# Optimization experiments

Hardware: AMD Instinct MI355X
Metric: run time of the kernel (lower is better)

The kernel has to match this reference:

```python
import jax, jax.numpy as jnp
import numpy as np

N = 8192
IOU_THRESH = 0.5
MAX_PROPOSALS = 1000


def setup_inputs() -> dict:
    key = jax.random.key(0)
    k1, k2, k3, k4 = jax.random.split(key, 4)
    # valid xyxy boxes inside a ~1000x1000 image, widths/heights in [1, 101)
    xy1 = jax.random.uniform(k1, (N, 2), dtype=jnp.float32) * 900.0
    wh = jax.random.uniform(k2, (N, 2), dtype=jnp.float32) * 100.0 + 1.0
    boxes = jnp.concatenate([xy1, xy1 + wh], axis=1)  # [N,4] xyxy
    scores = jax.random.uniform(k3, (N,), dtype=jnp.float32)
    return {"boxes": boxes, "scores": scores}


def _nms_keep(boxes, scores, thresh, max_proposals):
    # boxes: [N,4] xyxy (already sorted by descending score)
    x1, y1, x2, y2 = boxes[:, 0], boxes[:, 1], boxes[:, 2], boxes[:, 3]
    area = (x2 - x1) * (y2 - y1)  # [N]
    # pairwise IoU [N,N] (computed once; suppression loop gathers rows)
    xx1 = jnp.maximum(x1[:, None], x1[None, :])
    yy1 = jnp.maximum(y1[:, None], y1[None, :])
    xx2 = jnp.minimum(x2[:, None], x2[None, :])
    yy2 = jnp.minimum(y2[:, None], y2[None, :])
    inter = jnp.clip(xx2 - xx1, 0.0) * jnp.clip(yy2 - yy1, 0.0)
    iou = inter / (area[:, None] + area[None, :] - inter)
    n = boxes.shape[0]
    idx = jnp.arange(n)

    def body(i, keep):
        # box i (if still kept) suppresses later boxes with IoU > thresh
        suppress = keep[i] & (iou[i] > thresh) & (idx > i)
        return keep & ~suppress

    keep = jax.lax.fori_loop(0, n, body, jnp.ones((n,), dtype=bool))
    # truncate to max_proposals surviving boxes (in score order)
    keep = keep & (jnp.cumsum(keep.astype(jnp.int32)) <= max_proposals)
    return keep


def reference(boxes, scores):
    # sort by descending score (boxlist_nms sorts by score_field)
    order = jnp.argsort(-scores)
    b = boxes[order]          # [N,4]
    s = scores[order]         # [N]
    # keep mask is a discrete decision -> computed on stop_gradient inputs
    keep = _nms_keep(jax.lax.stop_gradient(b), jax.lax.stop_gradient(s),
                     IOU_THRESH, MAX_PROPOSALS)
    # fixed-shape output: [N,5] = (x1,y1,x2,y2,score), zeroed where suppressed
    out = jnp.concatenate([b, s[:, None]], axis=1) * keep[:, None].astype(b.dtype)
    return out
```

## Files before the change

### kernel.cpp

```cpp
#include <hip/hip_runtime.h>
#include <hip/hip_bf16.h>

#define N 8192
#define NW 128
#define GR 64
#define GROUPS 128
#define MAXP 1000
#define K_E 16
typedef unsigned long long u64;

__device__ float4 g_sboxes[N];
__device__ float  g_sscores[N];
__device__ u64    g_mask[(size_t)N * NW];
__device__ u64    g_diagT[N];
__device__ unsigned short g_elist[N][K_E];
__device__ int    g_ecnt[N];
__device__ u64    g_keep[NW];
__device__ int    g_wpre[NW];

__global__ __launch_bounds__(256) void k_rank2(const float4* __restrict__ boxes,
                                               const float* __restrict__ scores) {
  __shared__ u64 lk[8][1025];
  const int t = threadIdx.x;
  if (blockIdx.x < 32) g_ecnt[blockIdx.x * 256 + t] = 0;
#pragma unroll
  for (int k = 0; k < 32; ++k) {
    int j = t + 256 * k;
    unsigned sb = __float_as_uint(scores[j]);
    lk[j >> 10][j & 1023] = ((u64)(sb ^ 0xFFFFFFFFu) << 32) | (unsigned)j;
  }
  __syncthreads();
  const int row = blockIdx.x * 32 + (t >> 3);
  const int seg = t & 7;
  unsigned sbr = __float_as_uint(scores[row]);
  const u64 ki = ((u64)(sbr ^ 0xFFFFFFFFu) << 32) | (unsigned)row;
  const u64* s = lk[seg];
  int cnt = 0;
#pragma unroll 8
  for (int j = 0; j < 1024; ++j) cnt += (s[j] < ki) ? 1 : 0;
  cnt += __shfl_xor(cnt, 1);
  cnt += __shfl_xor(cnt, 2);
  cnt += __shfl_xor(cnt, 4);
  if (seg == 0) {
    g_sboxes[cnt] = boxes[row];
    g_sscores[cnt] = scores[row];
  }
}

__global__ __launch_bounds__(256) void k_mask4() {
#pragma clang fp contract(off)
  const int col = blockIdx.x;
  const int rowq = blockIdx.y;
  if (col < rowq * 4) return;
  const int t = threadIdx.x;
  const int wv = t >> 6, lane = t & 63;
  const int jbase = col * 64;
  __shared__ float4 cb[64];
  __shared__ u64 sh[4][64];
  if (t < 64) cb[t] = g_sboxes[jbase + t];
  __syncthreads();
  const int row = rowq * 4 + wv;
  if (col < row) return;
  const int i = row * 64 + lane;
  float4 bi = g_sboxes[i];
  u64 ov = 0;
  for (int c = 0; c < 64; ++c) {
    float4 bj = cb[c];
    float xx1 = fmaxf(bi.x, bj.x);
    float yy1 = fmaxf(bi.y, bj.y);
    float xx2 = fminf(bi.z, bj.z);
    float yy2 = fminf(bi.w, bj.w);
    bool cand = (xx2 > xx1) && (yy2 > yy1);
    if (cand) ov |= (1ull << c);
  }
  if (col == row) ov &= (lane < 63) ? (~0ull << (lane + 1)) : 0ull;
  float areai = (bi.z - bi.x) * (bi.w - bi.y);
  u64 bits = 0;
  while (ov) {
    int c = __ffsll((long long)ov) - 1;
    ov &= ov - 1;
    float4 bj = cb[c];
    float xx1 = fmaxf(bi.x, bj.x);
    float yy1 = fmaxf(bi.y, bj.y);
    float xx2 = fminf(bi.z, bj.z);
    float yy2 = fminf(bi.w, bj.w);
    float ww = fmaxf(xx2 - xx1, 0.0f);
    float hh = fmaxf(yy2 - yy1, 0.0f);
    float inter = ww * hh;
    float areaj = (bj.z - bj.x) * (bj.w - bj.y);
    float uni = (areai + areaj) - inter;
    float iou = inter / uni;
    if (iou > 0.5f) bits |= (1ull << c);
  }
  if (bits) g_mask[(size_t)i * NW + col] = bits;
  u64 eb = bits;
  while (eb) {
    int c = __ffsll((long long)eb) - 1;
    eb &= eb - 1;
    int slot = atomicAdd(&g_ecnt[i], 1);
    if (slot < K_E) g_elist[i][slot] = (unsigned short)(jbase + c);
  }
  if (col == row) {
    sh[wv][lane] = bits;
    u64 colw = 0;
    for (int r = 0; r < 64; ++r) colw |= ((sh[wv][r] >> lane) & 1ull) << r;
    g_diagT[row * 64 + lane] = colw;
  }
}

__global__ __launch_bounds__(64) void k_serial6() {
  const int lane = threadIdx.x;
  __shared__ u64 remv[NW];
  __shared__ u64 keep_arr[NW];
  remv[lane] = 0; remv[lane + 64] = 0;
  keep_arr[lane] = 0; keep_arr[lane + 64] = 0;

  u64 tdA = g_diagT[lane];
  int cnA = g_ecnt[lane];
  const u64* el0 = (const u64*)&g_elist[lane][0];
  u64 eA0 = el0[0], eA1 = el0[1], eA2 = el0[2], eA3 = el0[3];

  int kept_total = 0;
  for (int g = 0; g < GROUPS; ++g) {
    u64 tdB = 0, eB0 = 0, eB1 = 0, eB2 = 0, eB3 = 0;
    int cnB = 0;
    if (g + 1 < GROUPS) {
      int base = (g + 1) * GR + lane;
      tdB = g_diagT[base];
      cnB = g_ecnt[base];
      const u64* el = (const u64*)&g_elist[base][0];
      eB0 = el[0]; eB1 = el[1]; eB2 = el[2]; eB3 = el[3];
    }

    u64 pend = ~remv[g];
    u64 keepm = 0;
    while (pend) {
      bool rdy = (((pend >> lane) & 1ull) != 0ull) && ((tdA & pend) == 0ull);
      u64 R = __ballot(rdy);
      keepm |= R;
      u64 S = __ballot((tdA & R) != 0ull);
      pend &= ~(R | S);
    }
    if (lane == 0) keep_arr[g] = keepm;

    if ((keepm >> lane) & 1ull) {
      int cnt = cnA < K_E ? cnA : K_E;
      const u64 ew0 = eA0, ew1 = eA1, ew2 = eA2, ew3 = eA3;
#define SCAT(W, Q)                                                     \
      _Pragma("unroll")                                                \
      for (int b = 0; b < 4; ++b) {                                    \
        int s = (Q) * 4 + b;                                           \
        if (s < cnt) {                                                 \
          int j = (int)(((W) >> (16 * b)) & 0xFFFFull);                \
          atomicOr(&remv[j >> 6], 1ull << (j & 63));                   \
        }                                                              \
      }
      SCAT(ew0, 0) SCAT(ew1, 1) SCAT(ew2, 2) SCAT(ew3, 3)
#undef SCAT
    }
    u64 ovf = __ballot((((keepm >> lane) & 1ull) != 0ull) && (cnA > K_E));
    while (ovf) {
      int rr = __ffsll((long long)ovf) - 1;
      ovf &= ovf - 1;
      const u64* rowp = g_mask + (size_t)(g * GR + rr) * NW;
      int w0 = g + lane, w1 = g + 64 + lane;
      u64 a0 = (w0 < NW) ? rowp[w0] : 0ull;
      u64 a1 = (w1 < NW) ? rowp[w1] : 0ull;
      if (a0) atomicOr(&remv[w0], a0);
      if (a1) atomicOr(&remv[w1], a1);
    }

    kept_total += __popcll(keepm);
    if (kept_total >= MAXP) break;

    tdA = tdB; cnA = cnB;
    eA0 = eB0; eA1 = eB1; eA2 = eB2; eA3 = eB3;
  }

  u64 k0 = keep_arr[2 * lane];
  u64 k1 = keep_arr[2 * lane + 1];
  g_keep[2 * lane] = k0;
  g_keep[2 * lane + 1] = k1;
  int pc0 = __popcll(k0);
  int s = pc0 + __popcll(k1);
  int ex = s;
  for (int d = 1; d < 64; d <<= 1) {
    int t2 = __shfl_up(ex, d);
    if (lane >= d) ex += t2;
  }
  ex -= s;
  g_wpre[2 * lane] = ex;
  g_wpre[2 * lane + 1] = ex + pc0;
}

__global__ __launch_bounds__(256) void k_out(float* __restrict__ out) {
  int i = blockIdx.x * 256 + threadIdx.x;
  int w = i >> 6, b = i & 63;
  u64 kw = g_keep[w];
  int before = g_wpre[w] + (b ? __popcll(kw << (64 - b)) : 0);
  bool k = (((kw >> b) & 1ull) != 0ull) && (before < MAXP);
  float m = k ? 1.0f : 0.0f;
  float4 bx = g_sboxes[i];
  float sc = g_sscores[i];
  out[i * 5 + 0] = bx.x * m;
  out[i * 5 + 1] = bx.y * m;
  out[i * 5 + 2] = bx.z * m;
  out[i * 5 + 3] = bx.w * m;
  out[i * 5 + 4] = sc * m;
}

extern "C" void kernel_launch(void* const* d_in, const int* in_sizes, int n_in,
                              void* d_out, int out_size, void* d_ws, size_t ws_size,
                              hipStream_t stream) {
  const float4* boxes = (const float4*)d_in[0];
  const float*  scores = (const float*)d_in[1];
  float* out = (float*)d_out;

  hipLaunchKernelGGL(k_rank2,   dim3(N / 32),     dim3(256), 0, stream, boxes, scores);
  hipLaunchKernelGGL(k_mask4,   dim3(NW, NW / 4), dim3(256), 0, stream);
  hipLaunchKernelGGL(k_serial6, dim3(1),          dim3(64),  0, stream);
  hipLaunchKernelGGL(k_out,     dim3(N / 256),    dim3(256), 0, stream, out);
}
```

Measured before the change: 59.49 us.

## Compute mask for leading 48 groups first, fall back to full NMS only if needed

The IoU mask is first built only for the top 3072 score-sorted boxes, and the serial NMS runs over those groups. If 1000 boxes are kept within that prefix, the output is written directly. Otherwise a guarded full-mask kernel and full serial pass run as a fallback. The output write is also fused into the serial kernel, which drops the separate k_out launch. The cost is two extra launches that exit early, and a 256-thread single-block output loop in place of a 32-block grid.

```diff
diff --git a/kernel.cpp b/kernel.cpp
--- a/kernel.cpp
+++ b/kernel.cpp
@@ -5,6 +5,7 @@
 #define NW 128
 #define GR 64
 #define GROUPS 128
+#define CGR 48
 #define MAXP 1000
 #define K_E 16
 typedef unsigned long long u64;
@@ -13,16 +14,16 @@
 __device__ float  g_sscores[N];
 __device__ u64    g_mask[(size_t)N * NW];
 __device__ u64    g_diagT[N];
-__device__ unsigned short g_elist[N][K_E];
+__device__ __attribute__((aligned(8))) unsigned short g_elist[N][K_E];
 __device__ int    g_ecnt[N];
-__device__ u64    g_keep[NW];
-__device__ int    g_wpre[NW];
+__device__ int    g_need_full;
 
 __global__ __launch_bounds__(256) void k_rank2(const float4* __restrict__ boxes,
                                                const float* __restrict__ scores) {
   __shared__ u64 lk[8][1025];
   const int t = threadIdx.x;
   if (blockIdx.x < 32) g_ecnt[blockIdx.x * 256 + t] = 0;
+  if (blockIdx.x == 0 && t == 0) g_need_full = 0;
 #pragma unroll
   for (int k = 0; k < 32; ++k) {
     int j = t + 256 * k;
@@ -47,21 +48,11 @@
   }
 }
 
-__global__ __launch_bounds__(256) void k_mask4() {
+__device__ __forceinline__ void tile_work(int col, int row, int lane,
+                                          const float4* cb, u64* sh) {
 #pragma clang fp contract(off)
-  const int col = blockIdx.x;
-  const int rowq = blockIdx.y;
-  if (col < rowq * 4) return;
-  const int t = threadIdx.x;
-  const int wv = t >> 6, lane = t & 63;
+  const int i = row * 64 + lane;
   const int jbase = col * 64;
-  __shared__ float4 cb[64];
-  __shared__ u64 sh[4][64];
-  if (t < 64) cb[t] = g_sboxes[jbase + t];
-  __syncthreads();
-  const int row = rowq * 4 + wv;
-  if (col < row) return;
-  const int i = row * 64 + lane;
   float4 bi = g_sboxes[i];
   u64 ov = 0;
   for (int c = 0; c < 64; ++c) {
@@ -101,112 +92,159 @@
     if (slot < K_E) g_elist[i][slot] = (unsigned short)(jbase + c);
   }
   if (col == row) {
-    sh[wv][lane] = bits;
+    sh[lane] = bits;
     u64 colw = 0;
-    for (int r = 0; r < 64; ++r) colw |= ((sh[wv][r] >> lane) & 1ull) << r;
+    for (int r = 0; r < 64; ++r) colw |= ((sh[r] >> lane) & 1ull) << r;
     g_diagT[row * 64 + lane] = colw;
   }
 }
 
-__global__ __launch_bounds__(64) void k_serial6() {
-  const int lane = threadIdx.x;
+__global__ __launch_bounds__(256) void k_maskc() {
+  const int col = blockIdx.x;
+  const int rowq = blockIdx.y;
+  if (col < rowq * 4) return;
+  const int t = threadIdx.x;
+  const int wv = t >> 6, lane = t & 63;
+  __shared__ float4 cb[64];
+  __shared__ u64 sh[4][64];
+  if (t < 64) cb[t] = g_sboxes[col * 64 + t];
+  __syncthreads();
+  const int row = rowq * 4 + wv;
+  if (col < row) return;
+  tile_work(col, row, lane, cb, sh[wv]);
+}
+
+__global__ __launch_bounds__(256) void k_maskr() {
+  if (g_need_full == 0) return;
+  const int col = blockIdx.x;
+  const int rowq = blockIdx.y;
+  if (col < rowq * 4) return;
+  const int t = threadIdx.x;
+  const int wv = t >> 6, lane = t & 63;
+  __shared__ float4 cb[64];
+  __shared__ u64 sh[4][64];
+  if (t < 64) cb[t] = g_sboxes[col * 64 + t];
+  __syncthreads();
+  const int row = rowq * 4 + wv;
+  if (col < row) return;
+  if (row < CGR && col < CGR) return;
+  tile_work(col, row, lane, cb, sh[wv]);
+}
+
+template<int GLIM, bool GUARDED>
+__device__ __forceinline__ void serial_body(float* __restrict__ out) {
+  if (GUARDED && g_need_full == 0) return;
+  const int t = threadIdx.x;
+  const int wave = t >> 6, lane = t & 63;
   __shared__ u64 remv[NW];
   __shared__ u64 keep_arr[NW];
-  remv[lane] = 0; remv[lane + 64] = 0;
-  keep_arr[lane] = 0; keep_arr[lane + 64] = 0;
-
-  u64 tdA = g_diagT[lane];
-  int cnA = g_ecnt[lane];
-  const u64* el0 = (const u64*)&g_elist[lane][0];
-  u64 eA0 = el0[0], eA1 = el0[1], eA2 = el0[2], eA3 = el0[3];
-
-  int kept_total = 0;
-  for (int g = 0; g < GROUPS; ++g) {
-    u64 tdB = 0, eB0 = 0, eB1 = 0, eB2 = 0, eB3 = 0;
-    int cnB = 0;
-    if (g + 1 < GROUPS) {
-      int base = (g + 1) * GR + lane;
-      tdB = g_diagT[base];
-      cnB = g_ecnt[base];
-      const u64* el = (const u64*)&g_elist[base][0];
-      eB0 = el[0]; eB1 = el[1]; eB2 = el[2]; eB3 = el[3];
+  __shared__ int wpre_s[NW];
+  __shared__ int done_s;
+  if (t < NW) { remv[t] = 0; keep_arr[t] = 0; }
+  __syncthreads();
+
+  if (wave == 0) {
+    u64 tdA = g_diagT[lane];
+    int cnA = g_ecnt[lane];
+    const u64* el0 = (const u64*)&g_elist[lane][0];
+    u64 eA0 = el0[0], eA1 = el0[1], eA2 = el0[2], eA3 = el0[3];
+
+    int kept_total = 0;
+    for (int g = 0; g < GLIM; ++g) {
+      u64 tdB = 0, eB0 = 0, eB1 = 0, eB2 = 0, eB3 = 0;
+      int cnB = 0;
+      if (g + 1 < GLIM) {
+        int base = (g + 1) * GR + lane;
+        tdB = g_diagT[base];
+        cnB = g_ecnt[base];
+        const u64* el = (const u64*)&g_elist[base][0];
+        eB0 = el[0]; eB1 = el[1]; eB2 = el[2]; eB3 = el[3];
+      }
+      u64 pend = ~remv[g];
+      u64 keepm = 0;
+      while (pend) {
+        bool rdy = (((pend >> lane) & 1ull) != 0ull) && ((tdA & pend) == 0ull);
+        u64 R = __ballot(rdy);
+        keepm |= R;
+        u64 S = __ballot((tdA & R) != 0ull);
+        pend &= ~(R | S);
+      }
+      if (lane == 0) keep_arr[g] = keepm;
+      if ((keepm >> lane) & 1ull) {
+        int cnt = cnA < K_E ? cnA : K_E;
+        const u64 ew0 = eA0, ew1 = eA1, ew2 = eA2, ew3 = eA3;
+#define SCAT(W, Q)                                                     \
+        _Pragma("unroll")                                              \
+        for (int b = 0; b < 4; ++b) {                                  \
+          int s = (Q) * 4 + b;                                         \
+          if (s < cnt) {                                               \
+            int j = (int)(((W) >> (16 * b)) & 0xFFFFull);              \
+            atomicOr(&remv[j >> 6], 1ull << (j & 63));                 \
+          }                                                            \
+        }
+        SCAT(ew0, 0) SCAT(ew1, 1) SCAT(ew2, 2) SCAT(ew3, 3)
+#undef SCAT
+      }
+      u64 ovf = __ballot((((keepm >> lane) & 1ull) != 0ull) && (cnA > K_E));
+      while (ovf) {
+        int rr = __ffsll((long long)ovf) - 1;
+        ovf &= ovf - 1;
+        const u64* rowp = g_mask + (size_t)(g * GR + rr) * NW;
+        int w0 = g + lane, w1 = g + 64 + lane;
+        u64 a0 = (w0 < NW) ? rowp[w0] : 0ull;
+        u64 a1 = (w1 < NW) ? rowp[w1] : 0ull;
+        if (a0) atomicOr(&remv[w0], a0);
+        if (a1) atomicOr(&remv[w1], a1);
+      }
+      kept_total += __popcll(keepm);
+      if (kept_total >= MAXP) break;
+      tdA = tdB; cnA = cnB;
+      eA0 = eB0; eA1 = eB1; eA2 = eB2; eA3 = eB3;
     }
-
-    u64 pend = ~remv[g];
-    u64 keepm = 0;
-    while (pend) {
-      bool rdy = (((pend >> lane) & 1ull) != 0ull) && ((tdA & pend) == 0ull);
-      u64 R = __ballot(rdy);
-      keepm |= R;
-      u64 S = __ballot((tdA & R) != 0ull);
-      pend &= ~(R | S);
+    if (lane == 0) done_s = (kept_total >= MAXP) ? 1 : 0;
+    u64 k0 = keep_arr[2 * lane];
+    u64 k1 = keep_arr[2 * lane + 1];
+    int pc0 = __popcll(k0);
+    int s = pc0 + __popcll(k1);
+    int ex = s;
+    for (int d = 1; d < 64; d <<= 1) {
+      int t2 = __shfl_up(ex, d);
+      if (lane >= d) ex += t2;
     }
-    if (lane == 0) keep_arr[g] = keepm;
-
-    if ((keepm >> lane) & 1ull) {
-      int cnt = cnA < K_E ? cnA : K_E;
-      const u64 ew0 = eA0, ew1 = eA1, ew2 = eA2, ew3 = eA3;
-#define SCAT(W, Q)                                                     \
-      _Pragma("unroll")                                                \
-      for (int b = 0; b < 4; ++b) {                                    \
-        int s = (Q) * 4 + b;                                           \
-        if (s < cnt) {                                                 \
-          int j = (int)(((W) >> (16 * b)) & 0xFFFFull);                \
-          atomicOr(&remv[j >> 6], 1ull << (j & 63));                   \
-        }                                                              \
-      }
-      SCAT(ew0, 0) SCAT(ew1, 1) SCAT(ew2, 2) SCAT(ew3, 3)
-#undef SCAT
+    ex -= s;
+    wpre_s[2 * lane] = ex;
+    wpre_s[2 * lane + 1] = ex + pc0;
+  }
+  __syncthreads();
+
+  if (!GUARDED) {
+    if (done_s == 0) {
+      if (t == 0) g_need_full = 1;
+      return;
     }
-    u64 ovf = __ballot((((keepm >> lane) & 1ull) != 0ull) && (cnA > K_E));
-    while (ovf) {
-      int rr = __ffsll((long long)ovf) - 1;
-      ovf &= ovf - 1;
-      const u64* rowp = g_mask + (size_t)(g * GR + rr) * NW;
-      int w0 = g + lane, w1 = g + 64 + lane;
-      u64 a0 = (w0 < NW) ? rowp[w0] : 0ull;
-      u64 a1 = (w1 < NW) ? rowp[w1] : 0ull;
-      if (a0) atomicOr(&remv[w0], a0);
-      if (a1) atomicOr(&remv[w1], a1);
-    }
-
-    kept_total += __popcll(keepm);
-    if (kept_total >= MAXP) break;
-
-    tdA = tdB; cnA = cnB;
-    eA0 = eB0; eA1 = eB1; eA2 = eB2; eA3 = eB3;
-  }
-
-  u64 k0 = keep_arr[2 * lane];
-  u64 k1 = keep_arr[2 * lane + 1];
-  g_keep[2 * lane] = k0;
-  g_keep[2 * lane + 1] = k1;
-  int pc0 = __popcll(k0);
-  int s = pc0 + __popcll(k1);
-  int ex = s;
-  for (int d = 1; d < 64; d <<= 1) {
-    int t2 = __shfl_up(ex, d);
-    if (lane >= d) ex += t2;
-  }
-  ex -= s;
-  g_wpre[2 * lane] = ex;
-  g_wpre[2 * lane + 1] = ex + pc0;
-}
-
-__global__ __launch_bounds__(256) void k_out(float* __restrict__ out) {
-  int i = blockIdx.x * 256 + threadIdx.x;
-  int w = i >> 6, b = i & 63;
-  u64 kw = g_keep[w];
-  int before = g_wpre[w] + (b ? __popcll(kw << (64 - b)) : 0);
-  bool k = (((kw >> b) & 1ull) != 0ull) && (before < MAXP);
-  float m = k ? 1.0f : 0.0f;
-  float4 bx = g_sboxes[i];
-  float sc = g_sscores[i];
-  out[i * 5 + 0] = bx.x * m;
-  out[i * 5 + 1] = bx.y * m;
-  out[i * 5 + 2] = bx.z * m;
-  out[i * 5 + 3] = bx.w * m;
-  out[i * 5 + 4] = sc * m;
+  }
+  for (int r = 0; r < N / 256; ++r) {
+    int i = r * 256 + t;
+    int w = i >> 6, b = i & 63;
+    u64 kw = keep_arr[w];
+    int before = wpre_s[w] + (b ? __popcll(kw << (64 - b)) : 0);
+    bool k = (((kw >> b) & 1ull) != 0ull) && (before < MAXP);
+    float m = k ? 1.0f : 0.0f;
+    float4 bx = g_sboxes[i];
+    float sc = g_sscores[i];
+    out[i * 5 + 0] = bx.x * m;
+    out[i * 5 + 1] = bx.y * m;
+    out[i * 5 + 2] = bx.z * m;
+    out[i * 5 + 3] = bx.w * m;
+    out[i * 5 + 4] = sc * m;
+  }
+}
+
+__global__ __launch_bounds__(256) void k_serialA(float* __restrict__ out) {
+  serial_body<CGR, false>(out);
+}
+__global__ __launch_bounds__(256) void k_serialF(float* __restrict__ out) {
+  serial_body<GROUPS, true>(out);
 }
 
 extern "C" void kernel_launch(void* const* d_in, const int* in_sizes, int n_in,
@@ -216,8 +254,9 @@
   const float*  scores = (const float*)d_in[1];
   float* out = (float*)d_out;
 
-  hipLaunchKernelGGL(k_rank2,   dim3(N / 32),     dim3(256), 0, stream, boxes, scores);
-  hipLaunchKernelGGL(k_mask4,   dim3(NW, NW / 4), dim3(256), 0, stream);
-  hipLaunchKernelGGL(k_serial6, dim3(1),          dim3(64),  0, stream);
-  hipLaunchKernelGGL(k_out,     dim3(N / 256),    dim3(256), 0, stream, out);
-}
+  hipLaunchKernelGGL(k_rank2,   dim3(N / 32),       dim3(256), 0, stream, boxes, scores);
+  hipLaunchKernelGGL(k_maskc,   dim3(CGR, CGR / 4), dim3(256), 0, stream);
+  hipLaunchKernelGGL(k_serialA, dim3(1),            dim3(256), 0, stream, out);
+  hipLaunchKernelGGL(k_maskr,   dim3(NW, NW / 4),   dim3(256), 0, stream);
+  hipLaunchKernelGGL(k_serialF, dim3(1),            dim3(256), 0, stream, out);
+}
```

New measurement: 55.53 us. -6.7%, faster.
